# Kernel optimization log

Hardware: AMD Instinct MI355X
Metric: run time of the kernel (lower is better)

## Reference

```python
import jax, jax.numpy as jnp
import numpy as np

N_HEAD = 16
POSE = 5
YAW = 1
END_X, END_Y = 18, 32
THETA = 1000.0
LN_EPS = 1e-5

def compute_axial_cis(dim, end_x, end_y, theta):
    # Axial 2D rotary: dim is per-head dim; dim//4 freqs per spatial axis.
    n = dim // 4
    freqs = 1.0 / (theta ** (jnp.arange(0, dim, 4)[:n].astype(jnp.float32) / dim))
    t = jnp.arange(end_x * end_y, dtype=jnp.float32)
    t_x = t % end_x
    t_y = jnp.floor(t / end_x)
    ang = jnp.concatenate([t_x[:, None] * freqs[None, :], t_y[:, None] * freqs[None, :]], axis=-1)  # [L, dim//2]
    return jnp.cos(ang), jnp.sin(ang)

def apply_rotary(x, cos, sin):
    # x: [B,H,L,D]; complex pairing = consecutive (even, odd) lanes, as in view_as_complex
    xe, xo = x[..., 0::2], x[..., 1::2]
    oe = xe * cos - xo * sin
    oo = xe * sin + xo * cos
    return jnp.stack([oe, oo], axis=-1).reshape(x.shape)

def layernorm(z, g, b):
    m = jnp.mean(z, axis=-1, keepdims=True)
    v = jnp.mean(jnp.square(z - m), axis=-1, keepdims=True)
    return (z - m) * jax.lax.rsqrt(v + LN_EPS) * g + b

def setup_inputs() -> dict:
    key = jax.random.key(0)
    ks = jax.random.split(key, 8)
    B, T, C = 16, 582, 1024
    x = jax.random.normal(ks[0], (B, T, C), dtype=jnp.float32)
    # additive causal mask (0 keep / -1e9 masked), as a float attn_mask
    causal = jnp.tril(jnp.ones((T, T), dtype=jnp.float32))
    attn_mask = jnp.broadcast_to(jnp.where(causal > 0, 0.0, -1e9), (B, T, T))
    s = 0.02
    Wq = jax.random.normal(ks[1], (C, C), dtype=jnp.float32) * s
    Wk = jax.random.normal(ks[2], (C, C), dtype=jnp.float32) * s
    Wv = jax.random.normal(ks[3], (C, C), dtype=jnp.float32) * s
    Wo = jax.random.normal(ks[4], (C, C), dtype=jnp.float32) * s
    q_ln_g = jnp.ones((C,), jnp.float32); q_ln_b = jnp.zeros((C,), jnp.float32)
    k_ln_g = jnp.ones((C,), jnp.float32); k_ln_b = jnp.zeros((C,), jnp.float32)
    return {"x": x, "attn_mask": attn_mask, "Wq": Wq, "Wk": Wk, "Wv": Wv, "Wo": Wo,
            "q_ln_g": q_ln_g, "q_ln_b": q_ln_b, "k_ln_g": k_ln_g, "k_ln_b": k_ln_b}

def reference(x, attn_mask, Wq, Wk, Wv, Wo, q_ln_g, q_ln_b, k_ln_g, k_ln_b):
    B, T, C = x.shape
    H = N_HEAD
    D = C // H
    q = layernorm(x @ Wq.T, q_ln_g, q_ln_b)
    k = layernorm(x @ Wk.T, k_ln_g, k_ln_b)
    v = (x @ Wv.T).reshape(B, T, H, D).transpose(0, 2, 1, 3)
    q = q.reshape(B, T, H, D).transpose(0, 2, 1, 3)
    k = k.reshape(B, T, H, D).transpose(0, 2, 1, 3)
    prefix = POSE + YAW
    if T > prefix:  # static shape condition
        cos, sin = compute_axial_cis(D, END_X, END_Y, THETA)
        L = T - prefix
        cos, sin = cos[:L], sin[:L]  # [L, D//2]
        q = jnp.concatenate([q[:, :, :prefix], apply_rotary(q[:, :, prefix:], cos, sin)], axis=2)
        k = jnp.concatenate([k[:, :, :prefix], apply_rotary(k[:, :, prefix:], cos, sin)], axis=2)
    scale = 1.0 / jnp.sqrt(jnp.float32(D))
    scores = jnp.einsum("bhqd,bhkd->bhqk", q, k) * scale + attn_mask[:, None, :, :]
    att = jax.nn.softmax(scores, axis=-1)
    y = jnp.einsum("bhqk,bhkd->bhqd", att, v)
    y = y.transpose(0, 2, 1, 3).reshape(B, T, C)
    return y @ Wo.T
```

## Files before the change

### kernel.cpp

```cpp
#include <hip/hip_runtime.h>
#include <hip/hip_bf16.h>

typedef short bf16x8 __attribute__((ext_vector_type(8)));
typedef short bf16x4 __attribute__((ext_vector_type(4)));
typedef float f32x4  __attribute__((ext_vector_type(4)));

#define LDP 72

__device__ __forceinline__ float bits2f(short u) {
  return __uint_as_float(((unsigned int)(unsigned short)u) << 16);
}
__device__ __forceinline__ short f2bits(float f) {
  __hip_bfloat16 h = __float2bfloat16(f);
  return *reinterpret_cast<short*>(&h);
}
__device__ __forceinline__ void gld16(const short* g, short* l) {
  __builtin_amdgcn_global_load_lds(
      (const __attribute__((address_space(1))) void*)g,
      (__attribute__((address_space(3))) void*)l, 16, 0, 0);
}

__global__ __launch_bounds__(256)
void cvt_x_kernel(const float* __restrict__ src, short* __restrict__ dst, long n) {
  long i = ((long)blockIdx.x * 256 + threadIdx.x) * 4;
  if (i + 3 < n) {
    float4 v = *(const float4*)(src + i);
    bf16x4 o;
    o[0] = f2bits(v.x); o[1] = f2bits(v.y); o[2] = f2bits(v.z); o[3] = f2bits(v.w);
    *(bf16x4*)(dst + i) = o;
  }
}

__global__ __launch_bounds__(256)
void cvt_w_kernel(const float* __restrict__ w0, const float* __restrict__ w1,
                  const float* __restrict__ w2, const float* __restrict__ w3,
                  short* __restrict__ dst) {
  long i = ((long)blockIdx.x * 256 + threadIdx.x) * 4;
  int sel = (int)(i >> 20);
  const float* s = (sel == 0) ? w0 : (sel == 1) ? w1 : (sel == 2) ? w2 : w3;
  long off = i & ((1L << 20) - 1);
  float4 v = *(const float4*)(s + off);
  bf16x4 o;
  o[0] = f2bits(v.x); o[1] = f2bits(v.y); o[2] = f2bits(v.z); o[3] = f2bits(v.w);
  *(bf16x4*)(dst + i) = o;
}

template<int MODE>
__global__ __launch_bounds__(256)
void gemm_nt(const short* __restrict__ A, const short* __restrict__ Bm,
             float* __restrict__ OutF, short* __restrict__ Oq,
             short* __restrict__ Ok, short* __restrict__ Ov,
             int M, int K, int N, int T, int TPAD) {
  __shared__ short As[128 * 64];
  __shared__ short Bs[128 * 64];
  const int tid = threadIdx.x;
  const int w = tid >> 6, l = tid & 63;
  const int wr = w >> 1, wc = w & 1;
  const int lg = l >> 4, lo = l & 15;
  const long row0 = (long)blockIdx.x * 128;
  const long col0 = (long)blockIdx.y * 128;

  const short* pa[4]; const short* pb[4]; short* la[4]; short* lb[4];
#pragma unroll
  for (int j = 0; j < 4; ++j) {
    const int c = w * 4 + j;
    const int off = c * 1024 + l * 16;
    const int row = off >> 7;
    const int lc  = (off & 127) ^ ((row & 7) << 4);
    long ga = row0 + row; if (ga > M - 1) ga = M - 1;
    pa[j] = &A[ga * K + (lc >> 1)];
    pb[j] = &Bm[(col0 + row) * K + (lc >> 1)];
    la[j] = &As[c * 512];
    lb[j] = &Bs[c * 512];
  }

  f32x4 acc[4][4] = {};

  for (int kt = 0; kt < K; kt += 64) {
    __syncthreads();
#pragma unroll
    for (int j = 0; j < 4; ++j) {
      gld16(pa[j] + kt, la[j]);
      gld16(pb[j] + kt, lb[j]);
    }
    __syncthreads();
    bf16x8 af[4][2], bfr[4][2];
#pragma unroll
    for (int mi = 0; mi < 4; ++mi)
#pragma unroll
      for (int ks = 0; ks < 2; ++ks) {
        int pe = (ks * 32 + lg * 8) ^ ((lo & 7) << 3);
        af[mi][ks] = *(const bf16x8*)(&As[(wr * 64 + mi * 16 + lo) * 64 + pe]);
      }
#pragma unroll
    for (int ni = 0; ni < 4; ++ni)
#pragma unroll
      for (int ks = 0; ks < 2; ++ks) {
        int pe = (ks * 32 + lg * 8) ^ ((lo & 7) << 3);
        bfr[ni][ks] = *(const bf16x8*)(&Bs[(wc * 64 + ni * 16 + lo) * 64 + pe]);
      }
#pragma unroll
    for (int mi = 0; mi < 4; ++mi)
#pragma unroll
      for (int ni = 0; ni < 4; ++ni)
#pragma unroll
        for (int ks = 0; ks < 2; ++ks)
          acc[mi][ni] = __builtin_amdgcn_mfma_f32_16x16x32_bf16(af[mi][ks], bfr[ni][ks], acc[mi][ni], 0, 0, 0);
  }

#pragma unroll
  for (int mi = 0; mi < 4; ++mi) {
#pragma unroll
    for (int r = 0; r < 4; ++r) {
      long m = row0 + wr * 64 + mi * 16 + lg * 4 + r;
      if (m >= M) continue;
#pragma unroll
      for (int ni = 0; ni < 4; ++ni) {
        long n = col0 + wc * 64 + ni * 16 + lo;
        float v = acc[mi][ni][r];
        if constexpr (MODE == 2) {
          OutF[m * (long)N + n] = v;
        } else {
          if (n < 1024) {
            Oq[m * 1024 + n] = f2bits(v);
          } else if (n < 2048) {
            Ok[m * 1024 + (n - 1024)] = f2bits(v);
          } else {
            long b = m / T, t = m - b * T;
            long nn = n - 2048, h = nn >> 6, d = nn & 63;
            Ov[((b * 16 + h) * 64 + d) * TPAD + t] = f2bits(v);
          }
        }
      }
    }
  }
}

__global__ __launch_bounds__(256)
void ln_rope_kernel(const short* __restrict__ qpre, const short* __restrict__ kpre,
                    const float* __restrict__ qg, const float* __restrict__ qb2,
                    const float* __restrict__ kg, const float* __restrict__ kb2,
                    short* __restrict__ qa, short* __restrict__ ka, int T) {
  const int row = blockIdx.x;
  const short* in; const float *g, *be; short* out;
  if (blockIdx.y == 0) { in = qpre; g = qg; be = qb2; out = qa; }
  else                 { in = kpre; g = kg; be = kb2; out = ka; }
  const int tid = threadIdx.x;
  const int c0 = tid * 4;

  bf16x4 xv = *(const bf16x4*)(&in[(long)row * 1024 + c0]);
  float xf[4];
  float s = 0.f, sq = 0.f;
#pragma unroll
  for (int i = 0; i < 4; ++i) { xf[i] = bits2f(xv[i]); s += xf[i]; sq += xf[i] * xf[i]; }
#pragma unroll
  for (int o = 1; o < 64; o <<= 1) { s += __shfl_xor(s, o); sq += __shfl_xor(sq, o); }
  __shared__ float red[8];
  const int w = tid >> 6, l = tid & 63;
  if (l == 0) { red[w] = s; red[4 + w] = sq; }
  __syncthreads();
  s  = red[0] + red[1] + red[2] + red[3];
  sq = red[4] + red[5] + red[6] + red[7];
  const float mean = s * (1.0f / 1024.0f);
  const float var  = sq * (1.0f / 1024.0f) - mean * mean;
  const float rstd = rsqrtf(var + 1e-5f);

  float4 gv = *(const float4*)(&g[c0]);
  float4 bv = *(const float4*)(&be[c0]);
  float z[4];
  z[0] = (xf[0] - mean) * rstd * gv.x + bv.x;
  z[1] = (xf[1] - mean) * rstd * gv.y + bv.y;
  z[2] = (xf[2] - mean) * rstd * gv.z + bv.z;
  z[3] = (xf[3] - mean) * rstd * gv.w + bv.w;

  const int t = row % T;
  const int p = t - 6;
  if (p >= 0) {
    const float tx = (float)(p % 18);
    const float ty = (float)(p / 18);
    const int jbase = (c0 & 63) >> 1;
#pragma unroll
    for (int q2 = 0; q2 < 2; ++q2) {
      const int jj = jbase + q2;
      const int i  = jj & 15;
      const float freq = exp2f(-(float)i * 0.6228615177913804f);
      const float ang  = ((jj < 16) ? tx : ty) * freq;
      float sv, cv;
      sincosf(ang, &sv, &cv);
      const float xe = z[q2 * 2], xo = z[q2 * 2 + 1];
      z[q2 * 2]     = xe * cv - xo * sv;
      z[q2 * 2 + 1] = xe * sv + xo * cv;
    }
  }
  const long b = row / T;
  const int h = c0 >> 6, d = c0 & 63;
  bf16x4 ov;
#pragma unroll
  for (int i = 0; i < 4; ++i) ov[i] = f2bits(z[i]);
  *(bf16x4*)(&out[(((b * 16 + h) * T) + t) * 64 + d]) = ov;
}

__global__ __launch_bounds__(256)
void attn_kernel(const short* __restrict__ Q, const short* __restrict__ Kk,
                 const short* __restrict__ Vt, short* __restrict__ Y,
                 int T, int TPAD) {
  __shared__ short QP[64 * LDP];
  __shared__ short Ks[64 * LDP];
  __shared__ short Vs[64 * LDP];
  const int tid = threadIdx.x;
  const int w = tid >> 6, l = tid & 63, lg = l >> 4, lo = l & 15;
  const int qb = gridDim.x - 1 - blockIdx.x;
  const int bh = blockIdx.y;
  const int b = bh >> 4, h = bh & 15;
  const long qbase = (long)bh * T * 64;
  short* Qs = QP;
  short* Ps = QP + w * 16 * LDP;

  const int r0 = tid >> 3, c0s = (tid & 7) * 8;
  const int r1 = r0 + 32, c1s = c0s;

#pragma unroll
  for (int j = 0; j < 2; ++j) {
    int ch = tid + j * 256;
    int r = ch >> 3, c = (ch & 7) * 8;
    int t = qb * 64 + r; if (t > T - 1) t = T - 1;
    *(bf16x8*)(&Qs[r * LDP + c]) = *(const bf16x8*)(&Q[qbase + (long)t * 64 + c]);
  }
  __syncthreads();
  bf16x8 qf[2];
  qf[0] = *(const bf16x8*)(&Qs[(w * 16 + lo) * LDP + lg * 8]);
  qf[1] = *(const bf16x8*)(&Qs[(w * 16 + lo) * LDP + 32 + lg * 8]);

  float mrow[4], lsum[4];
  f32x4 oacc[4] = {};
#pragma unroll
  for (int r = 0; r < 4; ++r) { mrow[r] = -3e38f; lsum[r] = 0.f; }
  const float SCL = 0.125f * 1.44269504f;
  const int nkt = qb + 1;

  bf16x8 kreg[2], vreg[2];
  const long vbase = (long)bh * 64;
  auto LOADKV = [&](int kt) {
    kreg[0] = *(const bf16x8*)(&Kk[qbase + (long)(kt * 64 + r0) * 64 + c0s]);
    kreg[1] = *(const bf16x8*)(&Kk[qbase + (long)(kt * 64 + r1) * 64 + c1s]);
    vreg[0] = *(const bf16x8*)(&Vt[(vbase + r0) * TPAD + kt * 64 + c0s]);
    vreg[1] = *(const bf16x8*)(&Vt[(vbase + r1) * TPAD + kt * 64 + c1s]);
  };
  LOADKV(0);

  for (int kt = 0; kt < nkt; ++kt) {
    __syncthreads();
    *(bf16x8*)(&Ks[r0 * LDP + c0s]) = kreg[0];
    *(bf16x8*)(&Ks[r1 * LDP + c1s]) = kreg[1];
    *(bf16x8*)(&Vs[r0 * LDP + c0s]) = vreg[0];
    *(bf16x8*)(&Vs[r1 * LDP + c1s]) = vreg[1];
    __syncthreads();
    if (kt + 1 < nkt) LOADKV(kt + 1);

    f32x4 sf[4] = {};
#pragma unroll
    for (int ni = 0; ni < 4; ++ni)
#pragma unroll
      for (int kk = 0; kk < 2; ++kk) {
        bf16x8 kfr = *(const bf16x8*)(&Ks[(ni * 16 + lo) * LDP + kk * 32 + lg * 8]);
        sf[ni] = __builtin_amdgcn_mfma_f32_16x16x32_bf16(qf[kk], kfr, sf[ni], 0, 0, 0);
      }

    float pm[4][4], tmax[4];
#pragma unroll
    for (int r = 0; r < 4; ++r) tmax[r] = -3e38f;
#pragma unroll
    for (int ni = 0; ni < 4; ++ni)
#pragma unroll
      for (int r = 0; r < 4; ++r) {
        int key  = kt * 64 + ni * 16 + lo;
        int qrow = qb * 64 + w * 16 + lg * 4 + r;
        float sv = sf[ni][r] * SCL;
        if (key > qrow || key >= T) sv = -3e38f;
        pm[ni][r] = sv;
        tmax[r] = fmaxf(tmax[r], sv);
      }
#pragma unroll
    for (int r = 0; r < 4; ++r)
#pragma unroll
      for (int o = 1; o < 16; o <<= 1) tmax[r] = fmaxf(tmax[r], __shfl_xor(tmax[r], o));

    bool need = !__all(tmax[0] <= mrow[0] && tmax[1] <= mrow[1] &&
                       tmax[2] <= mrow[2] && tmax[3] <= mrow[3]);
    if (need) {
#pragma unroll
      for (int r = 0; r < 4; ++r) {
        float mn = fmaxf(mrow[r], tmax[r]);
        float fsc = exp2f(mrow[r] - mn);
        mrow[r] = mn;
        lsum[r] *= fsc;
#pragma unroll
        for (int ni = 0; ni < 4; ++ni) oacc[ni][r] *= fsc;
      }
    }
    float psum[4] = {0.f, 0.f, 0.f, 0.f};
#pragma unroll
    for (int ni = 0; ni < 4; ++ni)
#pragma unroll
      for (int r = 0; r < 4; ++r) {
        float pv = exp2f(pm[ni][r] - mrow[r]);
        pm[ni][r] = pv;
        psum[r] += pv;
      }
#pragma unroll
    for (int r = 0; r < 4; ++r) {
#pragma unroll
      for (int o = 1; o < 16; o <<= 1) psum[r] += __shfl_xor(psum[r], o);
      lsum[r] += psum[r];
    }

#pragma unroll
    for (int ni = 0; ni < 4; ++ni)
#pragma unroll
      for (int r = 0; r < 4; ++r)
        Ps[(lg * 4 + r) * LDP + ni * 16 + lo] = f2bits(pm[ni][r]);

#pragma unroll
    for (int kk = 0; kk < 2; ++kk) {
      bf16x8 pf = *(const bf16x8*)(&Ps[lo * LDP + kk * 32 + lg * 8]);
#pragma unroll
      for (int ni = 0; ni < 4; ++ni) {
        bf16x8 vf = *(const bf16x8*)(&Vs[(ni * 16 + lo) * LDP + kk * 32 + lg * 8]);
        oacc[ni] = __builtin_amdgcn_mfma_f32_16x16x32_bf16(pf, vf, oacc[ni], 0, 0, 0);
      }
    }
  }

#pragma unroll
  for (int r = 0; r < 4; ++r) {
    int tq = qb * 64 + w * 16 + lg * 4 + r;
    if (tq >= T) continue;
    float inv = 1.0f / lsum[r];
#pragma unroll
    for (int ni = 0; ni < 4; ++ni) {
      float o = oacc[ni][r] * inv;
      Y[((long)b * T + tq) * 1024 + h * 64 + ni * 16 + lo] = f2bits(o);
    }
  }
}

extern "C" void kernel_launch(void* const* d_in, const int* in_sizes, int n_in,
                              void* d_out, int out_size, void* d_ws, size_t ws_size,
                              hipStream_t stream) {
  const float* x   = (const float*)d_in[0];
  const float* Wq  = (const float*)d_in[2];
  const float* Wk  = (const float*)d_in[3];
  const float* Wv  = (const float*)d_in[4];
  const float* Wo  = (const float*)d_in[5];
  const float* qg  = (const float*)d_in[6];
  const float* qb2 = (const float*)d_in[7];
  const float* kg  = (const float*)d_in[8];
  const float* kb2 = (const float*)d_in[9];

  const int B = 16, T = 582, C = 1024;
  const int M = B * T;
  const int TPAD = 584;

  short* ws = (short*)d_ws;
  const long E  = (long)M * C;
  const long EV = (long)B * 16 * 64 * TPAD;
  short* xb   = ws;
  short* qpre = ws + E;
  short* kpre = ws + 2 * E;
  short* ka   = ws + 3 * E;
  short* vat  = ws + 4 * E;
  short* wb   = ws + 4 * E + EV + 1024;
  short* qa   = xb;
  short* y    = qpre;
  float* out  = (float*)d_out;
  (void)ws_size; (void)in_sizes; (void)n_in; (void)out_size;

  const long WE = 1L << 20;

  cvt_x_kernel<<<(int)(E / 4 / 256), 256, 0, stream>>>(x, xb, E);
  cvt_w_kernel<<<(int)(4 * WE / 4 / 256), 256, 0, stream>>>(Wq, Wk, Wv, Wo, wb);

  dim3 gqkv((M + 127) / 128, 3072 / 128);
  gemm_nt<3><<<gqkv, 256, 0, stream>>>(xb, wb, nullptr, qpre, kpre, vat, M, C, 3072, T, TPAD);
  ln_rope_kernel<<<dim3(M, 2), 256, 0, stream>>>(qpre, kpre, qg, qb2, kg, kb2, qa, ka, T);
  attn_kernel<<<dim3((T + 63) / 64, B * 16), 256, 0, stream>>>(qa, ka, vat, y, T, TPAD);
  dim3 gout((M + 127) / 128, C / 128);
  gemm_nt<2><<<gout, 256, 0, stream>>>(y, wb + 3 * WE, out, nullptr, nullptr, nullptr, M, C, C, T, TPAD);
}
```

Before: 259.9 us.

## Load attention K/V fragments straight from global and remap GEMM tiles per XCD

The attention kernel no longer stages Q, K and V tiles through shared memory behind block-wide barriers. Each wave now loads its MFMA fragments directly from global memory, and only the per-wave P tile stays in LDS. The projection GEMM also remaps block indices so that tiles sharing rows or columns land on the same XCD, aiming for better L2 reuse. In exchange, each wave fetches K/V redundantly and there is no register prefetch for the next tile, so load latency may be exposed. The Q row clamp is also dropped, so tail blocks read past T.

```diff
diff --git a/kernel.cpp b/kernel.cpp
--- a/kernel.cpp
+++ b/kernel.cpp
@@ -57,21 +57,38 @@
   const int w = tid >> 6, l = tid & 63;
   const int wr = w >> 1, wc = w & 1;
   const int lg = l >> 4, lo = l & 15;
-  const long row0 = (long)blockIdx.x * 128;
-  const long col0 = (long)blockIdx.y * 128;
+
+  const int R = gridDim.x, C2 = gridDim.y;
+  const int d = blockIdx.y * R + blockIdx.x;
+  int r, c;
+  if ((R & 7) == 1 && (C2 & 7) == 0) {
+    const int x = d & 7, i = d >> 3;
+    const int C8 = C2 >> 3;
+    const int chunk = R * C8;
+    const int b9 = R >> 3;
+    const int rows0 = b9 + 1;
+    if (x == 0) { c = i / rows0; r = i % rows0; }
+    else {
+      const int nb = b9 * C2;
+      if (i < nb) { c = i / b9; r = rows0 + (x - 1) * b9 + i % b9; }
+      else { int p = chunk + (x - 1) * C8 + (i - nb); c = p / rows0; r = p % rows0; }
+    }
+  } else { r = blockIdx.x; c = blockIdx.y; }
+  const long row0 = (long)r * 128;
+  const long col0 = (long)c * 128;
 
   const short* pa[4]; const short* pb[4]; short* la[4]; short* lb[4];
 #pragma unroll
   for (int j = 0; j < 4; ++j) {
-    const int c = w * 4 + j;
-    const int off = c * 1024 + l * 16;
+    const int ch = w * 4 + j;
+    const int off = ch * 1024 + l * 16;
     const int row = off >> 7;
     const int lc  = (off & 127) ^ ((row & 7) << 4);
     long ga = row0 + row; if (ga > M - 1) ga = M - 1;
     pa[j] = &A[ga * K + (lc >> 1)];
     pb[j] = &Bm[(col0 + row) * K + (lc >> 1)];
-    la[j] = &As[c * 512];
-    lb[j] = &Bs[c * 512];
+    la[j] = &As[ch * 512];
+    lb[j] = &Bs[ch * 512];
   }
 
   f32x4 acc[4][4] = {};
@@ -111,13 +128,13 @@
 #pragma unroll
   for (int mi = 0; mi < 4; ++mi) {
 #pragma unroll
-    for (int r = 0; r < 4; ++r) {
-      long m = row0 + wr * 64 + mi * 16 + lg * 4 + r;
+    for (int rr = 0; rr < 4; ++rr) {
+      long m = row0 + wr * 64 + mi * 16 + lg * 4 + rr;
       if (m >= M) continue;
 #pragma unroll
       for (int ni = 0; ni < 4; ++ni) {
         long n = col0 + wc * 64 + ni * 16 + lo;
-        float v = acc[mi][ni][r];
+        float v = acc[mi][ni][rr];
         if constexpr (MODE == 2) {
           OutF[m * (long)N + n] = v;
         } else {
@@ -127,8 +144,8 @@
             Ok[m * 1024 + (n - 1024)] = f2bits(v);
           } else {
             long b = m / T, t = m - b * T;
-            long nn = n - 2048, h = nn >> 6, d = nn & 63;
-            Ov[((b * 16 + h) * 64 + d) * TPAD + t] = f2bits(v);
+            long nn = n - 2048, h = nn >> 6, dd = nn & 63;
+            Ov[((b * 16 + h) * 64 + dd) * TPAD + t] = f2bits(v);
           }
         }
       }
@@ -204,32 +221,20 @@
 void attn_kernel(const short* __restrict__ Q, const short* __restrict__ Kk,
                  const short* __restrict__ Vt, short* __restrict__ Y,
                  int T, int TPAD) {
-  __shared__ short QP[64 * LDP];
-  __shared__ short Ks[64 * LDP];
-  __shared__ short Vs[64 * LDP];
+  __shared__ short Ps[4][16 * LDP];
   const int tid = threadIdx.x;
   const int w = tid >> 6, l = tid & 63, lg = l >> 4, lo = l & 15;
   const int qb = gridDim.x - 1 - blockIdx.x;
   const int bh = blockIdx.y;
   const int b = bh >> 4, h = bh & 15;
   const long qbase = (long)bh * T * 64;
-  short* Qs = QP;
-  short* Ps = QP + w * 16 * LDP;
-
-  const int r0 = tid >> 3, c0s = (tid & 7) * 8;
-  const int r1 = r0 + 32, c1s = c0s;
-
-#pragma unroll
-  for (int j = 0; j < 2; ++j) {
-    int ch = tid + j * 256;
-    int r = ch >> 3, c = (ch & 7) * 8;
-    int t = qb * 64 + r; if (t > T - 1) t = T - 1;
-    *(bf16x8*)(&Qs[r * LDP + c]) = *(const bf16x8*)(&Q[qbase + (long)t * 64 + c]);
-  }
-  __syncthreads();
+  const long vbase = (long)bh * 64;
+  short* Pw = &Ps[w][0];
+
+  const long qrow_l = qb * 64 + w * 16 + lo;
   bf16x8 qf[2];
-  qf[0] = *(const bf16x8*)(&Qs[(w * 16 + lo) * LDP + lg * 8]);
-  qf[1] = *(const bf16x8*)(&Qs[(w * 16 + lo) * LDP + 32 + lg * 8]);
+  qf[0] = *(const bf16x8*)(&Q[qbase + qrow_l * 64 + lg * 8]);
+  qf[1] = *(const bf16x8*)(&Q[qbase + qrow_l * 64 + 32 + lg * 8]);
 
   float mrow[4], lsum[4];
   f32x4 oacc[4] = {};
@@ -238,33 +243,25 @@
   const float SCL = 0.125f * 1.44269504f;
   const int nkt = qb + 1;
 
-  bf16x8 kreg[2], vreg[2];
-  const long vbase = (long)bh * 64;
-  auto LOADKV = [&](int kt) {
-    kreg[0] = *(const bf16x8*)(&Kk[qbase + (long)(kt * 64 + r0) * 64 + c0s]);
-    kreg[1] = *(const bf16x8*)(&Kk[qbase + (long)(kt * 64 + r1) * 64 + c1s]);
-    vreg[0] = *(const bf16x8*)(&Vt[(vbase + r0) * TPAD + kt * 64 + c0s]);
-    vreg[1] = *(const bf16x8*)(&Vt[(vbase + r1) * TPAD + kt * 64 + c1s]);
-  };
-  LOADKV(0);
-
   for (int kt = 0; kt < nkt; ++kt) {
-    __syncthreads();
-    *(bf16x8*)(&Ks[r0 * LDP + c0s]) = kreg[0];
-    *(bf16x8*)(&Ks[r1 * LDP + c1s]) = kreg[1];
-    *(bf16x8*)(&Vs[r0 * LDP + c0s]) = vreg[0];
-    *(bf16x8*)(&Vs[r1 * LDP + c1s]) = vreg[1];
-    __syncthreads();
-    if (kt + 1 < nkt) LOADKV(kt + 1);
+    bf16x8 kfr[4][2], vf[4][2];
+#pragma unroll
+    for (int ni = 0; ni < 4; ++ni)
+#pragma unroll
+      for (int kk = 0; kk < 2; ++kk)
+        kfr[ni][kk] = *(const bf16x8*)(&Kk[qbase + (long)(kt * 64 + ni * 16 + lo) * 64 + kk * 32 + lg * 8]);
+#pragma unroll
+    for (int ni = 0; ni < 4; ++ni)
+#pragma unroll
+      for (int kk = 0; kk < 2; ++kk)
+        vf[ni][kk] = *(const bf16x8*)(&Vt[(vbase + ni * 16 + lo) * TPAD + kt * 64 + kk * 32 + lg * 8]);
 
     f32x4 sf[4] = {};
 #pragma unroll
     for (int ni = 0; ni < 4; ++ni)
 #pragma unroll
-      for (int kk = 0; kk < 2; ++kk) {
-        bf16x8 kfr = *(const bf16x8*)(&Ks[(ni * 16 + lo) * LDP + kk * 32 + lg * 8]);
-        sf[ni] = __builtin_amdgcn_mfma_f32_16x16x32_bf16(qf[kk], kfr, sf[ni], 0, 0, 0);
-      }
+      for (int kk = 0; kk < 2; ++kk)
+        sf[ni] = __builtin_amdgcn_mfma_f32_16x16x32_bf16(qf[kk], kfr[ni][kk], sf[ni], 0, 0, 0);
 
     float pm[4][4], tmax[4];
 #pragma unroll
@@ -318,16 +315,14 @@
     for (int ni = 0; ni < 4; ++ni)
 #pragma unroll
       for (int r = 0; r < 4; ++r)
-        Ps[(lg * 4 + r) * LDP + ni * 16 + lo] = f2bits(pm[ni][r]);
+        Pw[(lg * 4 + r) * LDP + ni * 16 + lo] = f2bits(pm[ni][r]);
 
 #pragma unroll
     for (int kk = 0; kk < 2; ++kk) {
-      bf16x8 pf = *(const bf16x8*)(&Ps[lo * LDP + kk * 32 + lg * 8]);
-#pragma unroll
-      for (int ni = 0; ni < 4; ++ni) {
-        bf16x8 vf = *(const bf16x8*)(&Vs[(ni * 16 + lo) * LDP + kk * 32 + lg * 8]);
-        oacc[ni] = __builtin_amdgcn_mfma_f32_16x16x32_bf16(pf, vf, oacc[ni], 0, 0, 0);
-      }
+      bf16x8 pf = *(const bf16x8*)(&Pw[lo * LDP + kk * 32 + lg * 8]);
+#pragma unroll
+      for (int ni = 0; ni < 4; ++ni)
+        oacc[ni] = __builtin_amdgcn_mfma_f32_16x16x32_bf16(pf, vf[ni][kk], oacc[ni], 0, 0, 0);
     }
   }
 
```

After: 293.2 us. +12.8%, slower.
